# Performance work log

Hardware: AMD Instinct MI355X
Metric: run time of the kernel (lower is better)

## Reference

```python
import jax, jax.numpy as jnp
import numpy as np

ORDER = 2
BN_EPS = 1e-5

def setup_inputs() -> dict:
    key = jax.random.key(0)
    ks = jax.random.split(key, 8)
    B, N, L, H = 32, 512, 12, 64
    S = 2                      # support_len
    OUT = 64                   # out_dim
    M = ORDER * S * H          # einsum middle dim = 256
    x = jax.random.normal(ks[0], (B, N, L, H), dtype=jnp.float32)
    # row-scaled random diffusion matrices to keep multi-hop propagation stable
    support = jax.random.uniform(ks[1], (S, N, N), dtype=jnp.float32) / N
    scale = 1.0 / M
    weight = scale * jax.random.normal(ks[2], (L, M, OUT), dtype=jnp.float32)
    eps = jnp.zeros((1,), dtype=jnp.float32)
    gamma = jnp.ones((OUT,), dtype=jnp.float32)
    beta = jnp.zeros((OUT,), dtype=jnp.float32)
    w2 = jax.random.normal(ks[3], (OUT, OUT), dtype=jnp.float32) / np.sqrt(OUT)
    b2 = jnp.zeros((OUT,), dtype=jnp.float32)
    return {"x": x, "support": support, "weight": weight, "eps": eps,
            "gamma": gamma, "beta": beta, "w2": w2, "b2": b2}

def reference(x, support, weight, eps, gamma, beta, w2, b2):
    B, N, L, H = x.shape
    xv = x.reshape(B, N, L * H)            # [B,N,LH]
    res = []
    for i in range(support.shape[0]):      # small fixed loop over supports
        A = support[i]                     # [N,N]
        out = xv
        for _ in range(ORDER):
            out = (1.0 + eps) * out + jnp.einsum('nm,bmd->bnd', A, out)
            res.append(out)
    out = jnp.stack(res, axis=-1)          # [B,N,LH,K], K = order*support_len
    K = out.shape[-1]
    out = out.reshape(B, N, L, H * K)      # [B,N,L,M]
    out = jnp.einsum('bnlm,lmo->bno', out, weight)   # [B,N,OUT]
    # dropout is identity in eval mode
    C = out.shape[-1]
    flat = out.reshape(B * N, C)
    mean = flat.mean(axis=0)
    var = flat.var(axis=0)                 # biased, matching torch BN training
    normed = (flat - mean) * jax.lax.rsqrt(var + BN_EPS) * gamma + beta
    y = jax.nn.relu(normed.reshape(B, N, C))
    return jnp.einsum('bnc,oc->bno', y, w2) + b2
```

## Files before the change

kernel.cpp:

```cpp
#include <hip/hip_runtime.h>
#include <hip/hip_bf16.h>
#include <cstddef>
#include <cstdint>

#define B_   32
#define N_   512
#define D_   768
#define OUT_ 64
#define R_   (B_ * N_)

typedef unsigned short u16;
typedef __bf16 bf16x8 __attribute__((ext_vector_type(8)));
typedef float  f32x4  __attribute__((ext_vector_type(4)));
typedef unsigned short u16x8 __attribute__((ext_vector_type(8)));

__device__ __forceinline__ u16 f2bf(float f) {
    __hip_bfloat16 h = __float2bfloat16(f);
    return __builtin_bit_cast(u16, h);
}

__device__ __forceinline__ f32x4 mfma16(u16x8 a, u16x8 b, f32x4 c) {
    return __builtin_amdgcn_mfma_f32_16x16x32_bf16(
        __builtin_bit_cast(bf16x8, a), __builtin_bit_cast(bf16x8, b), c, 0, 0, 0);
}

__device__ __forceinline__ void gl2lds16(const void* g, void* l) {
    __builtin_amdgcn_global_load_lds(
        (const __attribute__((address_space(1))) unsigned int*)g,
        (__attribute__((address_space(3))) unsigned int*)l, 16, 0, 0);
}

__global__ __launch_bounds__(256) void prep(
    const float* __restrict__ x, const float* __restrict__ support,
    const float* __restrict__ weight, const float* __restrict__ epsp,
    u16* __restrict__ xb, u16* __restrict__ MallC, u16* __restrict__ MT,
    u16* __restrict__ Wt)
{
    const int blk = blockIdx.x, tid = threadIdx.x;
    __shared__ float t[32][33];
    if (blk < 6144) {
        int i = (blk * 256 + tid) * 8;
        f32x4 a = *(const f32x4*)(x + i);
        f32x4 b = *(const f32x4*)(x + i + 4);
        u16x8 o;
#pragma unroll
        for (int j = 0; j < 4; ++j) { o[j] = f2bf(a[j]); o[4 + j] = f2bf(b[j]); }
        *(u16x8*)(xb + i) = o;
    } else if (blk < 6656) {
        int local = blk - 6144;
        int s = local >> 8, rem = local & 255;
        int n0 = (rem >> 4) * 32, m0 = (rem & 15) * 32;
        const float f = 1.0f + epsp[0];
        const float* S = support + (size_t)s * 262144;
#pragma unroll
        for (int p = 0; p < 4; ++p) {
            int nl = p * 8 + (tid >> 5), ml = tid & 31;
            float v = S[(size_t)(n0 + nl) * 512 + m0 + ml];
            if (n0 + nl == m0 + ml) v += f;
            MallC[(size_t)(n0 + nl) * 2048 + s * 1024 + m0 + ml] = f2bf(v);
            t[nl][ml] = v;
        }
        __syncthreads();
#pragma unroll
        for (int p = 0; p < 4; ++p) {
            int ml = p * 8 + (tid >> 5), nl = tid & 31;
            MT[(size_t)s * 262144 + (size_t)(m0 + ml) * 512 + n0 + nl] = f2bf(t[nl][ml]);
        }
    } else {
        int idx = (blk - 6656) * 256 + tid;
        int k = idx / 49152, rem = idx % 49152;
        int o = rem / 768, d = rem % 768;
        int l = d >> 6, hh = d & 63;
        Wt[idx] = f2bf(weight[((size_t)l * 256 + hh * 4 + k) * 64 + o]);
    }
}

__global__ __launch_bounds__(256) void msq(
    const u16* __restrict__ MallC_in, const u16* __restrict__ MT,
    u16* __restrict__ MallC_out)
{
    __shared__ __align__(16) u16 sm[8192];
    u16* Ps = sm; u16* Qs = sm + 4096;
    const int tid = threadIdx.x, lane = tid & 63, wid = tid >> 6;
    const int wr = wid >> 1, wc = wid & 1;
    const int s = blockIdx.z, i0 = blockIdx.y * 128, j0 = blockIdx.x * 128;
    const int lrow = lane & 15, lk = (lane >> 4) * 8;

    const u16* gsrc[4]; u16* ldst[4];
#pragma unroll
    for (int t = 0; t < 4; ++t) {
        int idx = wid * 4 + t;
        if (idx < 8) { gsrc[t] = MallC_in + (size_t)(i0 + idx * 16 + lrow) * 2048 + s * 1024 + lk; ldst[t] = Ps + idx * 512; }
        else { int s2 = idx - 8; gsrc[t] = MT + (size_t)s * 262144 + (size_t)(j0 + s2 * 16 + lrow) * 512 + lk; ldst[t] = Qs + s2 * 512; }
    }
    f32x4 acc[4][4] = {};
    for (int k0 = 0; k0 < 512; k0 += 32) {
#pragma unroll
        for (int t = 0; t < 4; ++t) gl2lds16(gsrc[t], ldst[t]);
#pragma unroll
        for (int t = 0; t < 4; ++t) gsrc[t] += 32;
        __syncthreads();
        u16x8 af[4], bq[4];
#pragma unroll
        for (int f = 0; f < 4; ++f) af[f] = *(const u16x8*)(Ps + (wr * 4 + f) * 512 + lane * 8);
#pragma unroll
        for (int f = 0; f < 4; ++f) bq[f] = *(const u16x8*)(Qs + (wc * 4 + f) * 512 + lane * 8);
#pragma unroll
        for (int fi = 0; fi < 4; ++fi)
#pragma unroll
            for (int fj = 0; fj < 4; ++fj) acc[fi][fj] = mfma16(af[fi], bq[fj], acc[fi][fj]);
        __syncthreads();
    }
    const int q = lane >> 4;
#pragma unroll
    for (int fi = 0; fi < 4; ++fi)
#pragma unroll
        for (int fj = 0; fj < 4; ++fj)
#pragma unroll
            for (int r = 0; r < 4; ++r) {
                int n = i0 + wr * 64 + fi * 16 + q * 4 + r;
                int c = j0 + wc * 64 + fj * 16 + lrow;
                MallC_out[(size_t)n * 2048 + (2 * s + 1) * 512 + c] = f2bf(acc[fi][fj][r]);
            }
}

__global__ __launch_bounds__(256) void zgemm(
    const u16* __restrict__ Wt, const u16* __restrict__ xb, u16* __restrict__ Z)
{
    __shared__ __align__(16) u16 sm[9216];
    u16* As = sm; u16* Bs = sm + 2048;
    const int tid = threadIdx.x, lane = tid & 63, wid = tid >> 6;
    const int wr = wid >> 1, wc = wid & 1;
    const int j0 = blockIdx.x * 128, k = blockIdx.y;
    const int b = j0 >> 9, m0 = j0 & 511;
    const int lrow = lane & 15, lk = (lane >> 4) * 8;

    const u16* gsrc[3]; u16* ldst[3];
#pragma unroll
    for (int t = 0; t < 3; ++t) {
        int idx = wid * 3 + t;
        if (idx < 4) { gsrc[t] = Wt + (size_t)(k * 64 + idx * 16 + lrow) * 768 + lk; ldst[t] = As + idx * 512; }
        else { int s2 = idx - 4; gsrc[t] = xb + (size_t)(j0 + s2 * 16 + lrow) * 768 + lk; ldst[t] = Bs + s2 * 512; }
    }
    f32x4 acc[2][4] = {};
    for (int k0 = 0; k0 < 768; k0 += 32) {
#pragma unroll
        for (int t = 0; t < 3; ++t) gl2lds16(gsrc[t], ldst[t]);
#pragma unroll
        for (int t = 0; t < 3; ++t) gsrc[t] += 32;
        __syncthreads();
        u16x8 af[2], bq[4];
#pragma unroll
        for (int f = 0; f < 2; ++f) af[f] = *(const u16x8*)(As + (wr * 2 + f) * 512 + lane * 8);
#pragma unroll
        for (int f = 0; f < 4; ++f) bq[f] = *(const u16x8*)(Bs + (wc * 4 + f) * 512 + lane * 8);
#pragma unroll
        for (int fi = 0; fi < 2; ++fi)
#pragma unroll
            for (int fj = 0; fj < 4; ++fj) acc[fi][fj] = mfma16(af[fi], bq[fj], acc[fi][fj]);
        __syncthreads();
    }
    u16* Rw = sm + wid * 2304;
    const int q = lane >> 4;
#pragma unroll
    for (int fi = 0; fi < 2; ++fi)
#pragma unroll
        for (int fj = 0; fj < 4; ++fj)
#pragma unroll
            for (int r = 0; r < 4; ++r)
                Rw[(fi * 16 + q * 4 + r) * 72 + fj * 16 + lrow] = f2bf(acc[fi][fj][r]);
    __syncthreads();
#pragma unroll
    for (int p = 0; p < 4; ++p) {
        int row = p * 8 + (lane >> 3);
        int cc = (lane & 7) * 8;
        int o = wr * 32 + row;
        u16x8 v = *(const u16x8*)(Rw + row * 72 + cc);
        *(u16x8*)(Z + ((size_t)(b * 64 + o) * 4 + k) * 512 + m0 + wc * 64 + cc) = v;
    }
}

__global__ __launch_bounds__(256) void ysum(
    const u16* __restrict__ MallC, const u16* __restrict__ Z,
    float* __restrict__ Ysum, float* __restrict__ part)
{
    __shared__ __align__(16) char smem[43520];
    u16*   St = (u16*)smem;
    float* Rk = (float*)smem;
    float* vs = (float*)(smem + 34816);
    const int tid = threadIdx.x, lane = tid & 63, wid = tid >> 6;
    const int n0 = blockIdx.x * 32, b = blockIdx.y;
    const int lrow = lane & 15, lk = (lane >> 4) * 8;

    const u16* gsrc[6]; u16* ldst[6];
#pragma unroll
    for (int t = 0; t < 2; ++t) {
        gsrc[t] = MallC + (size_t)(n0 + t * 16 + lrow) * 2048 + wid * 512 + lk;
        ldst[t] = St + (wid * 6 + t) * 512;
    }
#pragma unroll
    for (int t = 0; t < 4; ++t) {
        gsrc[2 + t] = Z + (size_t)(b * 64 + t * 16 + lrow) * 2048 + wid * 512 + lk;
        ldst[2 + t] = St + (wid * 6 + 2 + t) * 512;
    }
    f32x4 acc[2][4] = {};
    for (int k0 = 0; k0 < 512; k0 += 32) {
#pragma unroll
        for (int t = 0; t < 6; ++t) gl2lds16(gsrc[t], ldst[t]);
#pragma unroll
        for (int t = 0; t < 6; ++t) gsrc[t] += 32;
        __syncthreads();
        u16x8 af[2], bq[4];
#pragma unroll
        for (int f = 0; f < 2; ++f) af[f] = *(const u16x8*)(St + (wid * 6 + f) * 512 + lane * 8);
#pragma unroll
        for (int f = 0; f < 4; ++f) bq[f] = *(const u16x8*)(St + (wid * 6 + 2 + f) * 512 + lane * 8);
#pragma unroll
        for (int fi = 0; fi < 2; ++fi)
#pragma unroll
            for (int fj = 0; fj < 4; ++fj) acc[fi][fj] = mfma16(af[fi], bq[fj], acc[fi][fj]);
        __syncthreads();
    }
    const int q = lane >> 4;
#pragma unroll
    for (int fi = 0; fi < 2; ++fi)
#pragma unroll
        for (int fj = 0; fj < 4; ++fj)
#pragma unroll
            for (int r = 0; r < 4; ++r)
                Rk[wid * 2176 + (fi * 16 + q * 4 + r) * 68 + fj * 16 + lrow] = acc[fi][fj][r];
    __syncthreads();
    {
        const int r = tid >> 3, c0 = (tid & 7) * 8;
        float v[8];
#pragma unroll
        for (int j = 0; j < 8; ++j) {
            v[j] = Rk[r * 68 + c0 + j] + Rk[2176 + r * 68 + c0 + j]
                 + Rk[4352 + r * 68 + c0 + j] + Rk[6528 + r * 68 + c0 + j];
            vs[r * 68 + c0 + j] = v[j];
        }
        float* dst = Ysum + ((size_t)(b * 512 + n0 + r)) * 64 + c0;
        f32x4 v0, v1;
#pragma unroll
        for (int j = 0; j < 4; ++j) { v0[j] = v[j]; v1[j] = v[4 + j]; }
        *(f32x4*)dst = v0;
        *(f32x4*)(dst + 4) = v1;
    }
    __syncthreads();
    if (tid < 64) {
        float s = 0.f, s2 = 0.f;
#pragma unroll
        for (int r2 = 0; r2 < 32; ++r2) {
            float u = vs[r2 * 68 + tid];
            s += u; s2 += u * u;
        }
        int blk = blockIdx.y * 16 + blockIdx.x;
        part[blk * 128 + tid]      = s;
        part[blk * 128 + 64 + tid] = s2;
    }
}

__global__ __launch_bounds__(256) void bn_final(
    const float* __restrict__ part, float* __restrict__ stats)
{
    const int tid = threadIdx.x;
    const int c = tid & 63, g = tid >> 6;
    float s = 0.f, s2 = 0.f;
    for (int b = g; b < 512; b += 4) {
        s  += part[b * 128 + c];
        s2 += part[b * 128 + 64 + c];
    }
    __shared__ float ls[4][64], ls2[4][64];
    ls[g][c] = s; ls2[g][c] = s2;
    __syncthreads();
    if (tid < 64) {
        float t = 0.f, t2 = 0.f;
#pragma unroll
        for (int g2 = 0; g2 < 4; ++g2) { t += ls[g2][tid]; t2 += ls2[g2][tid]; }
        float mean = t * (1.0f / R_);
        float var  = t2 * (1.0f / R_) - mean * mean;
        stats[tid]      = mean;
        stats[64 + tid] = rsqrtf(var + 1e-5f);
    }
}

__global__ __launch_bounds__(256) void bn_out(
    const float* __restrict__ Ysum, const float* __restrict__ stats,
    const float* __restrict__ gamma, const float* __restrict__ beta,
    const float* __restrict__ w2, const float* __restrict__ b2,
    float* __restrict__ out)
{
    __shared__ float ys[64 * 68];
    __shared__ float w2s[64 * 65];
    __shared__ float mn[64], rs[64], ga[64], be[64], bb[64];
    const int tid = threadIdx.x;
    const int r0 = blockIdx.x * 64;
#pragma unroll
    for (int i = 0; i < 16; ++i) {
        int idx = tid + i * 256;
        w2s[(idx >> 6) * 65 + (idx & 63)] = w2[idx];
    }
    if (tid < 64) {
        mn[tid] = stats[tid]; rs[tid] = stats[64 + tid];
        ga[tid] = gamma[tid]; be[tid] = beta[tid]; bb[tid] = b2[tid];
    }
    __syncthreads();
    const int o = tid & 63, rg = tid >> 6;
#pragma unroll
    for (int p = 0; p < 16; ++p) {
        int rl = p * 4 + rg;
        float v = Ysum[(size_t)(r0 + rl) * 64 + o];
        v = (v - mn[o]) * rs[o] * ga[o] + be[o];
        ys[o * 68 + rl] = fmaxf(v, 0.f);
    }
    __syncthreads();
    float acc[16];
#pragma unroll
    for (int j = 0; j < 16; ++j) acc[j] = bb[o];
    for (int c = 0; c < 64; ++c) {
        float wv = w2s[o * 65 + c];
        const float* yr = ys + c * 68 + rg * 16;
        f32x4 y0 = *(const f32x4*)(yr);
        f32x4 y1 = *(const f32x4*)(yr + 4);
        f32x4 y2 = *(const f32x4*)(yr + 8);
        f32x4 y3 = *(const f32x4*)(yr + 12);
#pragma unroll
        for (int j = 0; j < 4; ++j) {
            acc[j]      = fmaf(wv, y0[j], acc[j]);
            acc[4 + j]  = fmaf(wv, y1[j], acc[4 + j]);
            acc[8 + j]  = fmaf(wv, y2[j], acc[8 + j]);
            acc[12 + j] = fmaf(wv, y3[j], acc[12 + j]);
        }
    }
#pragma unroll
    for (int j = 0; j < 16; ++j)
        out[(size_t)(r0 + rg * 16 + j) * OUT_ + o] = acc[j];
}

extern "C" void kernel_launch(void* const* d_in, const int* in_sizes, int n_in,
                              void* d_out, int out_size, void* d_ws, size_t ws_size,
                              hipStream_t stream)
{
    const float* x       = (const float*)d_in[0];
    const float* support = (const float*)d_in[1];
    const float* weight  = (const float*)d_in[2];
    const float* eps     = (const float*)d_in[3];
    const float* gamma   = (const float*)d_in[4];
    const float* beta    = (const float*)d_in[5];
    const float* w2      = (const float*)d_in[6];
    const float* b2      = (const float*)d_in[7];
    float* out = (float*)d_out;

    char* ws = (char*)d_ws;
    u16*   xb    = (u16*)(ws);
    u16*   MallC = (u16*)(ws + 25165824);
    u16*   MT    = (u16*)(ws + 27262976);
    u16*   Wt    = (u16*)(ws + 28311552);
    u16*   Z     = (u16*)(ws + 28704768);
    float* Ysum  = (float*)(ws + 37093376);
    float* part  = (float*)(ws + 41287680);
    float* stats = (float*)(ws + 41549824);

    prep    <<<7424,            256, 0, stream>>>(x, support, weight, eps, xb, MallC, MT, Wt);
    msq     <<<dim3(4, 4, 2),   256, 0, stream>>>(MallC, MT, MallC);
    zgemm   <<<dim3(128, 4),    256, 0, stream>>>(Wt, xb, Z);
    ysum    <<<dim3(16, 32),    256, 0, stream>>>(MallC, Z, Ysum, part);
    bn_final<<<1,               256, 0, stream>>>(part, stats);
    bn_out  <<<256,             256, 0, stream>>>(Ysum, stats, gamma, beta, w2, b2, out);
}
```

Measured before the change: 199.7 us.

## Merge square and Z GEMMs into one launch; fuse ysum with BN via grid barriers

The separate msq and zgemm kernels become a single launch with 288 blocks, where the block index picks which GEMM a block computes. Both use 128x128 tiles and stage two 32-wide k panels per sync. The ysum, bn_final and bn_out kernels become one kernel that splits K in two and writes partial Y halves. Two software grid barriers on atomic counters, reset in prep, then sequence the statistics reduction and the BN, ReLU and output projection inside that kernel. This removes three launches and their gaps, but relies on all 256 blocks being co-resident for the spin barriers to be safe.

After: 201.8 us. No clear change (+1.1%).

```diff
diff --git a/kernel.cpp b/kernel.cpp
--- a/kernel.cpp
+++ b/kernel.cpp
@@ -30,15 +30,27 @@
         (__attribute__((address_space(3))) unsigned int*)l, 16, 0, 0);
 }
 
+__device__ __forceinline__ void gridbar(int* cnt, int nblk) {
+    __syncthreads();
+    if (threadIdx.x == 0) {
+        __threadfence();
+        __hip_atomic_fetch_add(cnt, 1, __ATOMIC_ACQ_REL, __HIP_MEMORY_SCOPE_AGENT);
+        while (__hip_atomic_load(cnt, __ATOMIC_ACQUIRE, __HIP_MEMORY_SCOPE_AGENT) < nblk)
+            __builtin_amdgcn_s_sleep(2);
+    }
+    __syncthreads();
+}
+
 __global__ __launch_bounds__(256) void prep(
     const float* __restrict__ x, const float* __restrict__ support,
     const float* __restrict__ weight, const float* __restrict__ epsp,
     u16* __restrict__ xb, u16* __restrict__ MallC, u16* __restrict__ MT,
-    u16* __restrict__ Wt)
+    u16* __restrict__ Wt, int* __restrict__ cnt)
 {
     const int blk = blockIdx.x, tid = threadIdx.x;
     __shared__ float t[32][33];
     if (blk < 6144) {
+        if (blk == 0 && tid < 2) cnt[tid] = 0;
         int i = (blk * 256 + tid) * 8;
         f32x4 a = *(const f32x4*)(x + i);
         f32x4 b = *(const f32x4*)(x + i + 4);
@@ -75,266 +87,264 @@
     }
 }
 
-__global__ __launch_bounds__(256) void msq(
+__global__ __launch_bounds__(256) void zgemmsq(
+    const u16* __restrict__ Wt, const u16* __restrict__ xb,
     const u16* __restrict__ MallC_in, const u16* __restrict__ MT,
-    u16* __restrict__ MallC_out)
+    u16* __restrict__ Z, u16* __restrict__ MallC_out)
 {
-    __shared__ __align__(16) u16 sm[8192];
-    u16* Ps = sm; u16* Qs = sm + 4096;
+    __shared__ __align__(16) char smem[36864];
+    u16* St = (u16*)smem;
     const int tid = threadIdx.x, lane = tid & 63, wid = tid >> 6;
     const int wr = wid >> 1, wc = wid & 1;
-    const int s = blockIdx.z, i0 = blockIdx.y * 128, j0 = blockIdx.x * 128;
     const int lrow = lane & 15, lk = (lane >> 4) * 8;
-
-    const u16* gsrc[4]; u16* ldst[4];
-#pragma unroll
-    for (int t = 0; t < 4; ++t) {
-        int idx = wid * 4 + t;
-        if (idx < 8) { gsrc[t] = MallC_in + (size_t)(i0 + idx * 16 + lrow) * 2048 + s * 1024 + lk; ldst[t] = Ps + idx * 512; }
-        else { int s2 = idx - 8; gsrc[t] = MT + (size_t)s * 262144 + (size_t)(j0 + s2 * 16 + lrow) * 512 + lk; ldst[t] = Qs + s2 * 512; }
+    const int bid = blockIdx.x;
+
+    const u16 *Ab, *Bb;
+    int strA, strB, kIters, i0, j0, s = 0;
+    bool ismsq;
+    if (bid < 256) {
+        ismsq = false;
+        i0 = (bid >> 7) * 128; j0 = (bid & 127) * 128;
+        Ab = Wt; strA = 768; Bb = xb; strB = 768; kIters = 12;
+    } else {
+        ismsq = true;
+        int lb = bid - 256;
+        s = lb >> 4; int rem = lb & 15;
+        i0 = (rem >> 2) * 128; j0 = (rem & 3) * 128;
+        Ab = MallC_in + s * 1024; strA = 2048;
+        Bb = MT + (size_t)s * 262144; strB = 512; kIters = 8;
+    }
+
+    const u16* gsrc[8]; u16* ldst[8];
+#pragma unroll
+    for (int t = 0; t < 8; ++t) {
+        int idx = wid * 8 + t;
+        int pan = idx >> 4, q2 = idx & 15;
+        if (q2 < 8) {
+            gsrc[t] = Ab + (size_t)(i0 + q2 * 16 + lrow) * strA + pan * 32 + lk;
+            ldst[t] = St + pan * 8192 + q2 * 512;
+        } else {
+            gsrc[t] = Bb + (size_t)(j0 + (q2 - 8) * 16 + lrow) * strB + pan * 32 + lk;
+            ldst[t] = St + pan * 8192 + 4096 + (q2 - 8) * 512;
+        }
     }
     f32x4 acc[4][4] = {};
-    for (int k0 = 0; k0 < 512; k0 += 32) {
-#pragma unroll
-        for (int t = 0; t < 4; ++t) gl2lds16(gsrc[t], ldst[t]);
-#pragma unroll
-        for (int t = 0; t < 4; ++t) gsrc[t] += 32;
-        __syncthreads();
-        u16x8 af[4], bq[4];
-#pragma unroll
-        for (int f = 0; f < 4; ++f) af[f] = *(const u16x8*)(Ps + (wr * 4 + f) * 512 + lane * 8);
-#pragma unroll
-        for (int f = 0; f < 4; ++f) bq[f] = *(const u16x8*)(Qs + (wc * 4 + f) * 512 + lane * 8);
+    for (int kk = 0; kk < kIters; ++kk) {
+#pragma unroll
+        for (int t = 0; t < 8; ++t) gl2lds16(gsrc[t], ldst[t]);
+#pragma unroll
+        for (int t = 0; t < 8; ++t) gsrc[t] += 64;
+        __syncthreads();
+#pragma unroll
+        for (int pan = 0; pan < 2; ++pan) {
+            u16x8 af[4], bq[4];
+#pragma unroll
+            for (int f = 0; f < 4; ++f)
+                af[f] = *(const u16x8*)(St + pan * 8192 + (wr * 4 + f) * 512 + lane * 8);
+#pragma unroll
+            for (int f = 0; f < 4; ++f)
+                bq[f] = *(const u16x8*)(St + pan * 8192 + 4096 + (wc * 4 + f) * 512 + lane * 8);
+#pragma unroll
+            for (int fi = 0; fi < 4; ++fi)
+#pragma unroll
+                for (int fj = 0; fj < 4; ++fj)
+                    acc[fi][fj] = mfma16(af[fi], bq[fj], acc[fi][fj]);
+        }
+        __syncthreads();
+    }
+    const int q = lane >> 4;
+    if (!ismsq) {
+        u16* Rw = (u16*)smem + wid * 4608;
 #pragma unroll
         for (int fi = 0; fi < 4; ++fi)
 #pragma unroll
-            for (int fj = 0; fj < 4; ++fj) acc[fi][fj] = mfma16(af[fi], bq[fj], acc[fi][fj]);
-        __syncthreads();
-    }
-    const int q = lane >> 4;
-#pragma unroll
-    for (int fi = 0; fi < 4; ++fi)
-#pragma unroll
-        for (int fj = 0; fj < 4; ++fj)
-#pragma unroll
-            for (int r = 0; r < 4; ++r) {
-                int n = i0 + wr * 64 + fi * 16 + q * 4 + r;
-                int c = j0 + wc * 64 + fj * 16 + lrow;
-                MallC_out[(size_t)n * 2048 + (2 * s + 1) * 512 + c] = f2bf(acc[fi][fj][r]);
-            }
-}
-
-__global__ __launch_bounds__(256) void zgemm(
-    const u16* __restrict__ Wt, const u16* __restrict__ xb, u16* __restrict__ Z)
-{
-    __shared__ __align__(16) u16 sm[9216];
-    u16* As = sm; u16* Bs = sm + 2048;
-    const int tid = threadIdx.x, lane = tid & 63, wid = tid >> 6;
-    const int wr = wid >> 1, wc = wid & 1;
-    const int j0 = blockIdx.x * 128, k = blockIdx.y;
-    const int b = j0 >> 9, m0 = j0 & 511;
-    const int lrow = lane & 15, lk = (lane >> 4) * 8;
-
-    const u16* gsrc[3]; u16* ldst[3];
-#pragma unroll
-    for (int t = 0; t < 3; ++t) {
-        int idx = wid * 3 + t;
-        if (idx < 4) { gsrc[t] = Wt + (size_t)(k * 64 + idx * 16 + lrow) * 768 + lk; ldst[t] = As + idx * 512; }
-        else { int s2 = idx - 4; gsrc[t] = xb + (size_t)(j0 + s2 * 16 + lrow) * 768 + lk; ldst[t] = Bs + s2 * 512; }
-    }
-    f32x4 acc[2][4] = {};
-    for (int k0 = 0; k0 < 768; k0 += 32) {
-#pragma unroll
-        for (int t = 0; t < 3; ++t) gl2lds16(gsrc[t], ldst[t]);
-#pragma unroll
-        for (int t = 0; t < 3; ++t) gsrc[t] += 32;
-        __syncthreads();
-        u16x8 af[2], bq[4];
-#pragma unroll
-        for (int f = 0; f < 2; ++f) af[f] = *(const u16x8*)(As + (wr * 2 + f) * 512 + lane * 8);
-#pragma unroll
-        for (int f = 0; f < 4; ++f) bq[f] = *(const u16x8*)(Bs + (wc * 4 + f) * 512 + lane * 8);
-#pragma unroll
-        for (int fi = 0; fi < 2; ++fi)
-#pragma unroll
-            for (int fj = 0; fj < 4; ++fj) acc[fi][fj] = mfma16(af[fi], bq[fj], acc[fi][fj]);
-        __syncthreads();
-    }
-    u16* Rw = sm + wid * 2304;
-    const int q = lane >> 4;
-#pragma unroll
-    for (int fi = 0; fi < 2; ++fi)
-#pragma unroll
-        for (int fj = 0; fj < 4; ++fj)
-#pragma unroll
-            for (int r = 0; r < 4; ++r)
-                Rw[(fi * 16 + q * 4 + r) * 72 + fj * 16 + lrow] = f2bf(acc[fi][fj][r]);
-    __syncthreads();
-#pragma unroll
-    for (int p = 0; p < 4; ++p) {
-        int row = p * 8 + (lane >> 3);
-        int cc = (lane & 7) * 8;
-        int o = wr * 32 + row;
-        u16x8 v = *(const u16x8*)(Rw + row * 72 + cc);
-        *(u16x8*)(Z + ((size_t)(b * 64 + o) * 4 + k) * 512 + m0 + wc * 64 + cc) = v;
-    }
-}
-
-__global__ __launch_bounds__(256) void ysum(
+            for (int fj = 0; fj < 4; ++fj)
+#pragma unroll
+                for (int r = 0; r < 4; ++r)
+                    Rw[(fi * 16 + q * 4 + r) * 72 + fj * 16 + lrow] = f2bf(acc[fi][fj][r]);
+        __syncthreads();
+        const int k = (i0 >> 6) + wr;
+        const int b = j0 >> 9;
+        const int m0 = (j0 & 511) + wc * 64;
+#pragma unroll
+        for (int p = 0; p < 8; ++p) {
+            int row = p * 8 + (lane >> 3);
+            int cc = (lane & 7) * 8;
+            u16x8 v = *(const u16x8*)(Rw + row * 72 + cc);
+            *(u16x8*)(Z + (size_t)(b * 64 + row) * 2048 + k * 512 + m0 + cc) = v;
+        }
+    } else {
+#pragma unroll
+        for (int fi = 0; fi < 4; ++fi)
+#pragma unroll
+            for (int fj = 0; fj < 4; ++fj)
+#pragma unroll
+                for (int r = 0; r < 4; ++r) {
+                    int n = i0 + wr * 64 + fi * 16 + q * 4 + r;
+                    int c = j0 + wc * 64 + fj * 16 + lrow;
+                    MallC_out[(size_t)n * 2048 + (2 * s + 1) * 512 + c] = f2bf(acc[fi][fj][r]);
+                }
+    }
+}
+
+__global__ __launch_bounds__(256) void ysumbn(
     const u16* __restrict__ MallC, const u16* __restrict__ Z,
-    float* __restrict__ Ysum, float* __restrict__ part)
-{
-    __shared__ __align__(16) char smem[43520];
-    u16*   St = (u16*)smem;
-    float* Rk = (float*)smem;
-    float* vs = (float*)(smem + 34816);
-    const int tid = threadIdx.x, lane = tid & 63, wid = tid >> 6;
-    const int n0 = blockIdx.x * 32, b = blockIdx.y;
-    const int lrow = lane & 15, lk = (lane >> 4) * 8;
-
-    const u16* gsrc[6]; u16* ldst[6];
-#pragma unroll
-    for (int t = 0; t < 2; ++t) {
-        gsrc[t] = MallC + (size_t)(n0 + t * 16 + lrow) * 2048 + wid * 512 + lk;
-        ldst[t] = St + (wid * 6 + t) * 512;
-    }
-#pragma unroll
-    for (int t = 0; t < 4; ++t) {
-        gsrc[2 + t] = Z + (size_t)(b * 64 + t * 16 + lrow) * 2048 + wid * 512 + lk;
-        ldst[2 + t] = St + (wid * 6 + 2 + t) * 512;
-    }
-    f32x4 acc[2][4] = {};
-    for (int k0 = 0; k0 < 512; k0 += 32) {
-#pragma unroll
-        for (int t = 0; t < 6; ++t) gl2lds16(gsrc[t], ldst[t]);
-#pragma unroll
-        for (int t = 0; t < 6; ++t) gsrc[t] += 32;
-        __syncthreads();
-        u16x8 af[2], bq[4];
-#pragma unroll
-        for (int f = 0; f < 2; ++f) af[f] = *(const u16x8*)(St + (wid * 6 + f) * 512 + lane * 8);
-#pragma unroll
-        for (int f = 0; f < 4; ++f) bq[f] = *(const u16x8*)(St + (wid * 6 + 2 + f) * 512 + lane * 8);
-#pragma unroll
-        for (int fi = 0; fi < 2; ++fi)
-#pragma unroll
-            for (int fj = 0; fj < 4; ++fj) acc[fi][fj] = mfma16(af[fi], bq[fj], acc[fi][fj]);
-        __syncthreads();
-    }
-    const int q = lane >> 4;
-#pragma unroll
-    for (int fi = 0; fi < 2; ++fi)
-#pragma unroll
-        for (int fj = 0; fj < 4; ++fj)
-#pragma unroll
-            for (int r = 0; r < 4; ++r)
-                Rk[wid * 2176 + (fi * 16 + q * 4 + r) * 68 + fj * 16 + lrow] = acc[fi][fj][r];
-    __syncthreads();
-    {
-        const int r = tid >> 3, c0 = (tid & 7) * 8;
-        float v[8];
-#pragma unroll
-        for (int j = 0; j < 8; ++j) {
-            v[j] = Rk[r * 68 + c0 + j] + Rk[2176 + r * 68 + c0 + j]
-                 + Rk[4352 + r * 68 + c0 + j] + Rk[6528 + r * 68 + c0 + j];
-            vs[r * 68 + c0 + j] = v[j];
-        }
-        float* dst = Ysum + ((size_t)(b * 512 + n0 + r)) * 64 + c0;
-        f32x4 v0, v1;
-#pragma unroll
-        for (int j = 0; j < 4; ++j) { v0[j] = v[j]; v1[j] = v[4 + j]; }
-        *(f32x4*)dst = v0;
-        *(f32x4*)(dst + 4) = v1;
-    }
-    __syncthreads();
-    if (tid < 64) {
-        float s = 0.f, s2 = 0.f;
-#pragma unroll
-        for (int r2 = 0; r2 < 32; ++r2) {
-            float u = vs[r2 * 68 + tid];
-            s += u; s2 += u * u;
-        }
-        int blk = blockIdx.y * 16 + blockIdx.x;
-        part[blk * 128 + tid]      = s;
-        part[blk * 128 + 64 + tid] = s2;
-    }
-}
-
-__global__ __launch_bounds__(256) void bn_final(
-    const float* __restrict__ part, float* __restrict__ stats)
-{
-    const int tid = threadIdx.x;
-    const int c = tid & 63, g = tid >> 6;
-    float s = 0.f, s2 = 0.f;
-    for (int b = g; b < 512; b += 4) {
-        s  += part[b * 128 + c];
-        s2 += part[b * 128 + 64 + c];
-    }
-    __shared__ float ls[4][64], ls2[4][64];
-    ls[g][c] = s; ls2[g][c] = s2;
-    __syncthreads();
-    if (tid < 64) {
-        float t = 0.f, t2 = 0.f;
-#pragma unroll
-        for (int g2 = 0; g2 < 4; ++g2) { t += ls[g2][tid]; t2 += ls2[g2][tid]; }
-        float mean = t * (1.0f / R_);
-        float var  = t2 * (1.0f / R_) - mean * mean;
-        stats[tid]      = mean;
-        stats[64 + tid] = rsqrtf(var + 1e-5f);
-    }
-}
-
-__global__ __launch_bounds__(256) void bn_out(
-    const float* __restrict__ Ysum, const float* __restrict__ stats,
+    float* __restrict__ Yh, float* __restrict__ part, int* __restrict__ cnt,
     const float* __restrict__ gamma, const float* __restrict__ beta,
     const float* __restrict__ w2, const float* __restrict__ b2,
     float* __restrict__ out)
 {
-    __shared__ float ys[64 * 68];
-    __shared__ float w2s[64 * 65];
-    __shared__ float mn[64], rs[64], ga[64], be[64], bb[64];
-    const int tid = threadIdx.x;
-    const int r0 = blockIdx.x * 64;
+    __shared__ __align__(16) char smem[36864];
+    u16* St = (u16*)smem;
+    float* ys    = (float*)smem;
+    float* w2s   = (float*)(smem + 17408);
+    float* red   = (float*)(smem + 34048);
+    float* red2  = (float*)(smem + 35072);
+    float* stats = (float*)(smem + 36096);
+    const int tid = threadIdx.x, lane = tid & 63, wid = tid >> 6;
+    const int wr = wid >> 1, wc = wid & 1;
+    const int lrow = lane & 15, lk = (lane >> 4) * 8;
+    const int r0 = blockIdx.x * 128, ks = blockIdx.y;
+    const int b = blockIdx.x >> 2, n0 = r0 & 511;
+    const size_t km0 = (size_t)ks * 1024;
+
+    const u16* gsrc[6]; u16* ldst[6];
+#pragma unroll
+    for (int t = 0; t < 6; ++t) {
+        int idx = wid * 6 + t;
+        int pan = idx / 12, q2 = idx % 12;
+        if (q2 < 8) {
+            gsrc[t] = MallC + (size_t)(n0 + q2 * 16 + lrow) * 2048 + km0 + pan * 32 + lk;
+            ldst[t] = St + pan * 6144 + q2 * 512;
+        } else {
+            gsrc[t] = Z + (size_t)(b * 64 + (q2 - 8) * 16 + lrow) * 2048 + km0 + pan * 32 + lk;
+            ldst[t] = St + pan * 6144 + 4096 + (q2 - 8) * 512;
+        }
+    }
+    f32x4 acc[4][2] = {};
+    for (int kk = 0; kk < 16; ++kk) {
+#pragma unroll
+        for (int t = 0; t < 6; ++t) gl2lds16(gsrc[t], ldst[t]);
+#pragma unroll
+        for (int t = 0; t < 6; ++t) gsrc[t] += 64;
+        __syncthreads();
+#pragma unroll
+        for (int pan = 0; pan < 2; ++pan) {
+            u16x8 af[4], bq[2];
+#pragma unroll
+            for (int f = 0; f < 4; ++f)
+                af[f] = *(const u16x8*)(St + pan * 6144 + (wr * 4 + f) * 512 + lane * 8);
+#pragma unroll
+            for (int f = 0; f < 2; ++f)
+                bq[f] = *(const u16x8*)(St + pan * 6144 + 4096 + (wc * 2 + f) * 512 + lane * 8);
+#pragma unroll
+            for (int fi = 0; fi < 4; ++fi)
+#pragma unroll
+                for (int fj = 0; fj < 2; ++fj)
+                    acc[fi][fj] = mfma16(af[fi], bq[fj], acc[fi][fj]);
+        }
+        __syncthreads();
+    }
+    const int q = lane >> 4;
+    float* Yk = Yh + (size_t)ks * R_ * 64;
+#pragma unroll
+    for (int fi = 0; fi < 4; ++fi)
+#pragma unroll
+        for (int fj = 0; fj < 2; ++fj)
+#pragma unroll
+            for (int r = 0; r < 4; ++r) {
+                int rr = r0 + wr * 64 + fi * 16 + q * 4 + r;
+                int o  = wc * 32 + fj * 16 + lrow;
+                Yk[(size_t)rr * 64 + o] = acc[fi][fj][r];
+            }
+
+    gridbar(cnt, 256);
+
+    const int bid = blockIdx.y * 128 + blockIdx.x;
+    const int rb = bid * 64;
+    const int o = tid & 63, g = tid >> 6;
+    {
+        float s = 0.f, s2 = 0.f;
+#pragma unroll
+        for (int p = 0; p < 16; ++p) {
+            int rl = p * 4 + g;
+            size_t off = (size_t)(rb + rl) * 64 + o;
+            float v = Yh[off] + Yh[(size_t)R_ * 64 + off];
+            ys[o * 68 + rl] = v;
+            s += v; s2 += v * v;
+        }
+        red[g * 64 + o] = s; red2[g * 64 + o] = s2;
+    }
 #pragma unroll
     for (int i = 0; i < 16; ++i) {
         int idx = tid + i * 256;
         w2s[(idx >> 6) * 65 + (idx & 63)] = w2[idx];
     }
+    __syncthreads();
     if (tid < 64) {
-        mn[tid] = stats[tid]; rs[tid] = stats[64 + tid];
-        ga[tid] = gamma[tid]; be[tid] = beta[tid]; bb[tid] = b2[tid];
-    }
-    __syncthreads();
-    const int o = tid & 63, rg = tid >> 6;
-#pragma unroll
-    for (int p = 0; p < 16; ++p) {
-        int rl = p * 4 + rg;
-        float v = Ysum[(size_t)(r0 + rl) * 64 + o];
-        v = (v - mn[o]) * rs[o] * ga[o] + be[o];
-        ys[o * 68 + rl] = fmaxf(v, 0.f);
-    }
-    __syncthreads();
-    float acc[16];
-#pragma unroll
-    for (int j = 0; j < 16; ++j) acc[j] = bb[o];
-    for (int c = 0; c < 64; ++c) {
-        float wv = w2s[o * 65 + c];
-        const float* yr = ys + c * 68 + rg * 16;
-        f32x4 y0 = *(const f32x4*)(yr);
-        f32x4 y1 = *(const f32x4*)(yr + 4);
-        f32x4 y2 = *(const f32x4*)(yr + 8);
-        f32x4 y3 = *(const f32x4*)(yr + 12);
-#pragma unroll
-        for (int j = 0; j < 4; ++j) {
-            acc[j]      = fmaf(wv, y0[j], acc[j]);
-            acc[4 + j]  = fmaf(wv, y1[j], acc[4 + j]);
-            acc[8 + j]  = fmaf(wv, y2[j], acc[8 + j]);
-            acc[12 + j] = fmaf(wv, y3[j], acc[12 + j]);
-        }
-    }
-#pragma unroll
-    for (int j = 0; j < 16; ++j)
-        out[(size_t)(r0 + rg * 16 + j) * OUT_ + o] = acc[j];
+        float t0 = red[tid] + red[64 + tid] + red[128 + tid] + red[192 + tid];
+        float t2 = red2[tid] + red2[64 + tid] + red2[128 + tid] + red2[192 + tid];
+        part[bid * 128 + tid]      = t0;
+        part[bid * 128 + 64 + tid] = t2;
+    }
+
+    gridbar(cnt + 1, 256);
+
+    {
+        float s = 0.f, s2 = 0.f;
+        for (int p = g; p < 256; p += 4) {
+            s  += part[p * 128 + o];
+            s2 += part[p * 128 + 64 + o];
+        }
+        red[g * 64 + o] = s; red2[g * 64 + o] = s2;
+    }
+    __syncthreads();
+    if (tid < 64) {
+        float t0 = red[tid] + red[64 + tid] + red[128 + tid] + red[192 + tid];
+        float t2 = red2[tid] + red2[64 + tid] + red2[128 + tid] + red2[192 + tid];
+        float mean = t0 * (1.0f / R_);
+        float var  = t2 * (1.0f / R_) - mean * mean;
+        float rstd = rsqrtf(var + 1e-5f);
+        float a = rstd * gamma[tid];
+        stats[tid]      = a;
+        stats[64 + tid] = beta[tid] - mean * a;
+    }
+    __syncthreads();
+    {
+        float a = stats[o], sh = stats[64 + o];
+#pragma unroll
+        for (int p = 0; p < 16; ++p) {
+            int rl = p * 4 + g;
+            float v = ys[o * 68 + rl];
+            ys[o * 68 + rl] = fmaxf(fmaf(v, a, sh), 0.f);
+        }
+    }
+    __syncthreads();
+    {
+        const int rg = g;
+        float accs[16];
+        float bb = b2[o];
+#pragma unroll
+        for (int j = 0; j < 16; ++j) accs[j] = bb;
+        for (int c = 0; c < 64; ++c) {
+            float wv = w2s[o * 65 + c];
+            const float* yr = ys + c * 68 + rg * 16;
+            f32x4 y0 = *(const f32x4*)(yr);
+            f32x4 y1 = *(const f32x4*)(yr + 4);
+            f32x4 y2 = *(const f32x4*)(yr + 8);
+            f32x4 y3 = *(const f32x4*)(yr + 12);
+#pragma unroll
+            for (int j = 0; j < 4; ++j) {
+                accs[j]      = fmaf(wv, y0[j], accs[j]);
+                accs[4 + j]  = fmaf(wv, y1[j], accs[4 + j]);
+                accs[8 + j]  = fmaf(wv, y2[j], accs[8 + j]);
+                accs[12 + j] = fmaf(wv, y3[j], accs[12 + j]);
+            }
+        }
+#pragma unroll
+        for (int j = 0; j < 16; ++j)
+            out[(size_t)(rb + rg * 16 + j) * OUT_ + o] = accs[j];
+    }
 }
 
 extern "C" void kernel_launch(void* const* d_in, const int* in_sizes, int n_in,
@@ -357,14 +367,13 @@
     u16*   MT    = (u16*)(ws + 27262976);
     u16*   Wt    = (u16*)(ws + 28311552);
     u16*   Z     = (u16*)(ws + 28704768);
-    float* Ysum  = (float*)(ws + 37093376);
-    float* part  = (float*)(ws + 41287680);
-    float* stats = (float*)(ws + 41549824);
-
-    prep    <<<7424,            256, 0, stream>>>(x, support, weight, eps, xb, MallC, MT, Wt);
-    msq     <<<dim3(4, 4, 2),   256, 0, stream>>>(MallC, MT, MallC);
-    zgemm   <<<dim3(128, 4),    256, 0, stream>>>(Wt, xb, Z);
-    ysum    <<<dim3(16, 32),    256, 0, stream>>>(MallC, Z, Ysum, part);
-    bn_final<<<1,               256, 0, stream>>>(part, stats);
-    bn_out  <<<256,             256, 0, stream>>>(Ysum, stats, gamma, beta, w2, b2, out);
-}
+    float* Yh    = (float*)(ws + 37093376);
+    float* part  = (float*)(ws + 45481984);
+    int*   cnt   = (int*)(ws + 45613056);
+
+    prep   <<<7424,          256, 0, stream>>>(x, support, weight, eps,
+                                               xb, MallC, MT, Wt, cnt);
+    zgemmsq<<<288,           256, 0, stream>>>(Wt, xb, MallC, MT, Z, MallC);
+    ysumbn <<<dim3(128, 2),  256, 0, stream>>>(MallC, Z, Yh, part, cnt,
+                                               gamma, beta, w2, b2, out);
+}
```
